# Kernel tuning notes

Hardware: AMD Instinct MI355X
Metric: run time of the kernel (lower is better)

The kernel has to match this reference:

```python
import jax, jax.numpy as jnp
import numpy as np

VOCAB = 50257
D_MODEL = 256
HIDDEN = 512
NUM_CLASSES = 2
BATCH = 64
SEQ = 512
PAD_IDX = 0


def setup_inputs() -> dict:
    key = jax.random.key(0)
    ks = jax.random.split(key, 8)
    input_ids = jax.random.randint(ks[0], (BATCH, SEQ), 0, VOCAB)
    emb = jax.random.normal(ks[1], (VOCAB, D_MODEL), dtype=jnp.float32) * 0.02
    emb = emb.at[PAD_IDX].set(0.0)  # padding_idx row is zero
    s_x = 1.0 / np.sqrt(D_MODEL)
    s_h = 1.0 / np.sqrt(HIDDEN)
    Wx = jax.random.uniform(ks[2], (D_MODEL, 3 * HIDDEN), minval=-s_x, maxval=s_x)
    Wh = jax.random.uniform(ks[3], (HIDDEN, 3 * HIDDEN), minval=-s_h, maxval=s_h)
    bx = jax.random.uniform(ks[4], (3 * HIDDEN,), minval=-s_h, maxval=s_h)
    bh = jax.random.uniform(ks[5], (3 * HIDDEN,), minval=-s_h, maxval=s_h)
    Wo = jax.random.uniform(ks[6], (HIDDEN, NUM_CLASSES), minval=-s_h, maxval=s_h)
    bo = jax.random.uniform(ks[7], (NUM_CLASSES,), minval=-s_h, maxval=s_h)
    return {"input_ids": input_ids, "emb": emb, "Wx": Wx, "Wh": Wh,
            "bx": bx, "bh": bh, "Wo": Wo, "bo": bo}


def reference(input_ids, emb, Wx, Wh, bx, bh, Wo, bo):
    # Embedding lookup: [B, S, D]
    x = emb[input_ids]
    # Precompute input-side gate projections for all timesteps: [B, S, 3H]
    xg = jnp.einsum('bsd,dg->bsg', x, Wx) + bx
    H = Wh.shape[0]
    h0 = jnp.zeros((input_ids.shape[0], H), dtype=x.dtype)

    def step(h, xg_t):
        hg = h @ Wh + bh                    # [B, 3H]
        xr, xz, xn = jnp.split(xg_t, 3, axis=-1)
        hr, hz, hn = jnp.split(hg, 3, axis=-1)
        r = jax.nn.sigmoid(xr + hr)
        z = jax.nn.sigmoid(xz + hz)
        n = jnp.tanh(xn + r * hn)
        h_new = (1.0 - z) * n + z * h
        return h_new, None

    # scan over time; only the last hidden state feeds the classifier head
    h_last, _ = jax.lax.scan(step, h0, jnp.swapaxes(xg, 0, 1))
    # Dropout is identity in eval mode (p=0.5 at train time)
    logits = h_last @ Wo + bo               # [B, num_classes]
    return logits
```

## Files before the change

### kernel.cpp

```cpp
#include <hip/hip_runtime.h>
#include <hip/hip_bf16.h>

#define BATCH   64
#define SEQ     512
#define DMODEL  256
#define HIDDEN  512
#define G3      1536
#define NBLK    128
#define UPB     4
#define CPB     12
#define CHUNK   128
#define NCHUNK  4
#define HSLOT   (HIDDEN * BATCH)

typedef unsigned long long u64;
typedef unsigned int u32;

__global__ __launch_bounds__(512) void prep_wh(const float* __restrict__ Wh,
                                               float* __restrict__ whp) {
    int t = blockIdx.x * 512 + threadIdx.x;
    int k   = t & 511;
    int cb  = t >> 9;
    int c   = cb % 12;
    int blk = cb / 12;
    int u = c & 3, g = c >> 2;
    whp[t] = Wh[(long)k * G3 + g * HIDDEN + blk * UPB + u];
}

__global__ void init_flags(unsigned* flags) {
    __hip_atomic_store(&flags[threadIdx.x], 0u, __ATOMIC_RELAXED,
                       __HIP_MEMORY_SCOPE_AGENT);
}

__global__ __launch_bounds__(256) void xg_gemm(const int* __restrict__ ids,
                                               const float* __restrict__ emb,
                                               const float* __restrict__ Wx,
                                               const float* __restrict__ bx,
                                               float* __restrict__ xgC,
                                               int chunk) {
    __shared__ float Es[64][68];
    __shared__ float Ws[64][68];
    __shared__ int   sids[64];

    const int tid = threadIdx.x;
    const int nb = blockIdx.x;
    const int lt = blockIdx.y;
    const int s  = chunk * CHUNK + lt;
    const int tn = tid & 15;
    const int tm = tid >> 4;

    if (tid < 64) sids[tid] = ids[tid * SEQ + s];
    __syncthreads();

    float acc[4][4];
#pragma unroll
    for (int i = 0; i < 4; ++i)
#pragma unroll
        for (int j = 0; j < 4; ++j) acc[i][j] = 0.f;

    for (int kb = 0; kb < 256; kb += 64) {
#pragma unroll
        for (int p = 0; p < 4; ++p) {
            int b = p * 16 + tm;
            float4 av = *(const float4*)(emb + (long)sids[b] * DMODEL + kb + tn * 4);
            Es[tn * 4 + 0][b] = av.x;
            Es[tn * 4 + 1][b] = av.y;
            Es[tn * 4 + 2][b] = av.z;
            Es[tn * 4 + 3][b] = av.w;
            int krow = p * 16 + tm;
            float4 wv = *(const float4*)(Wx + (long)(kb + krow) * G3 + nb * 64 + tn * 4);
            *(float4*)&Ws[krow][tn * 4] = wv;
        }
        __syncthreads();
#pragma unroll
        for (int k = 0; k < 64; ++k) {
            float4 w4 = *(const float4*)&Ws[k][tm * 4];
            float4 e4 = *(const float4*)&Es[k][tn * 4];
            float ww[4] = {w4.x, w4.y, w4.z, w4.w};
            float ee[4] = {e4.x, e4.y, e4.z, e4.w};
#pragma unroll
            for (int i = 0; i < 4; ++i)
#pragma unroll
                for (int j = 0; j < 4; ++j)
                    acc[i][j] = fmaf(ww[i], ee[j], acc[i][j]);
        }
        __syncthreads();
    }

#pragma unroll
    for (int i = 0; i < 4; ++i) {
        int col = nb * 64 + tm * 4 + i;
        float bxi = bx[col];
        float4 o;
        o.x = acc[i][0] + bxi;
        o.y = acc[i][1] + bxi;
        o.z = acc[i][2] + bxi;
        o.w = acc[i][3] + bxi;
        *(float4*)(xgC + (long)col * (CHUNK * BATCH) + lt * 64 + tn * 4) = o;
    }
}

__global__ __launch_bounds__(512, 2) void gru_scan(const float* __restrict__ whp,
                                                   const float* __restrict__ xgC,
                                                   const float* __restrict__ bh,
                                                   float* hist,
                                                   unsigned* flags,
                                                   int chunk) {
    const int tid = threadIdx.x;
    const int blk = blockIdx.x;
    const int b   = tid & 63;
    const int wu  = __builtin_amdgcn_readfirstlane(tid >> 6);

    __shared__ float part[8][CPB][64];
    __shared__ float hl[UPB][64];

    const float* wb = whp + blk * (CPB * HIDDEN) + wu * 64;
    const int base = chunk * CHUNK;

    const int gu = tid >> 6;
    int jg = 0;
    float bhr = 0.f, bhz = 0.f, bhn = 0.f;
    const float* xr_p = nullptr; const float* xz_p = nullptr; const float* xn_p = nullptr;
    if (tid < 256) {
        jg  = blk * UPB + gu;
        bhr = bh[jg];
        bhz = bh[HIDDEN + jg];
        bhn = bh[2 * HIDDEN + jg];
        xr_p = xgC + (long)jg * (CHUNK * BATCH) + b;
        xz_p = xgC + (long)(HIDDEN + jg) * (CHUNK * BATCH) + b;
        xn_p = xgC + (long)(2 * HIDDEN + jg) * (CHUNK * BATCH) + b;
        hl[gu][b] = (chunk == 0) ? 0.f
                                 : hist[(long)blk * 256 + b * 4 + gu];
    }
    __syncthreads();

#pragma unroll 1
    for (int lt = 0; lt < CHUNK; ++lt) {
        const int t = base + lt;
        const float* hs = hist + (long)lt * HSLOT;
        float*       hw = hist + (long)((lt + 1) & (CHUNK - 1)) * HSLOT;

        float xr = 0.f, xz = 0.f, xn = 0.f, hprev = 0.f;
        if (tid < 256) {
            xr = xr_p[lt * 64];
            xz = xz_p[lt * 64];
            xn = xn_p[lt * 64];
            hprev = hl[gu][b];
        }

        if (t > 0) {
            const float4* hq4 = (const float4*)hs + (wu * 16) * 64 + b;
            float4 hv[16];
#pragma unroll
            for (int i = 0; i < 16; ++i)
                hv[i] = hq4[(long)i * 64];

            float acc[CPB];
#pragma unroll
            for (int c = 0; c < CPB; ++c) acc[c] = 0.f;
#pragma unroll
            for (int i = 0; i < 16; ++i) {
                const float he[4] = {hv[i].x, hv[i].y, hv[i].z, hv[i].w};
#pragma unroll
                for (int e = 0; e < 4; ++e) {
                    const float hvv = he[e];
                    const int kk = i * 4 + e;
#pragma unroll
                    for (int c = 0; c < CPB; ++c)
                        acc[c] = fmaf(hvv, wb[c * HIDDEN + kk], acc[c]);
                }
            }
#pragma unroll
            for (int c = 0; c < CPB; ++c) part[wu][c][b] = acc[c];
        } else {
#pragma unroll
            for (int c = 0; c < CPB; ++c) part[wu][c][b] = 0.f;
        }
        __syncthreads();

        if (tid < 256) {
            float hgr = bhr, hgz = bhz, hgn = bhn;
#pragma unroll
            for (int ww = 0; ww < 8; ++ww) {
                hgr += part[ww][gu][b];
                hgz += part[ww][4 + gu][b];
                hgn += part[ww][8 + gu][b];
            }
            float r  = 1.f / (1.f + expf(-(xr + hgr)));
            float z  = 1.f / (1.f + expf(-(xz + hgz)));
            float nn = tanhf(xn + r * hgn);
            hl[gu][b] = (1.f - z) * nn + z * hprev;
        }
        __syncthreads();

        if (tid < 128) {
            const int p = tid >> 6;
            u32 lo = __float_as_uint(hl[2 * p][b]);
            u32 hi = __float_as_uint(hl[2 * p + 1][b]);
            u64 pk = ((u64)hi << 32) | (u64)lo;
            __hip_atomic_store((u64*)(hw + (long)blk * 256 + b * 4 + 2 * p), pk,
                               __ATOMIC_RELAXED, __HIP_MEMORY_SCOPE_AGENT);
        }

        if (lt < CHUNK - 1) {
            __syncthreads();
            if (tid == 0)
                __hip_atomic_store(&flags[blk], (u32)(t + 1),
                                   __ATOMIC_RELAXED, __HIP_MEMORY_SCOPE_AGENT);
            if (wu == 0) {
                const u32 tgt = (u32)(t + 1);
                for (;;) {
                    u32 f0 = __hip_atomic_load(&flags[b], __ATOMIC_RELAXED,
                                               __HIP_MEMORY_SCOPE_AGENT);
                    u32 f1 = __hip_atomic_load(&flags[64 + b], __ATOMIC_RELAXED,
                                               __HIP_MEMORY_SCOPE_AGENT);
                    if (__all(f0 >= tgt && f1 >= tgt)) break;
                    __builtin_amdgcn_s_sleep(1);
                }
            }
            __syncthreads();
        }
    }
}

__global__ void head_kernel(const float* __restrict__ hist,
                            const float* __restrict__ Wo,
                            const float* __restrict__ bo,
                            float* __restrict__ out) {
    int tid = threadIdx.x;
    int b = tid >> 1, n = tid & 1;
    float acc = bo[n];
#pragma unroll 8
    for (int k = 0; k < HIDDEN; ++k)
        acc = fmaf(hist[(k >> 2) * 256 + b * 4 + (k & 3)], Wo[k * 2 + n], acc);
    out[b * 2 + n] = acc;
}

extern "C" void kernel_launch(void* const* d_in, const int* in_sizes, int n_in,
                              void* d_out, int out_size, void* d_ws, size_t ws_size,
                              hipStream_t stream) {
    (void)in_sizes; (void)n_in; (void)out_size; (void)ws_size;
    const int*   ids = (const int*)  d_in[0];
    const float* emb = (const float*)d_in[1];
    const float* Wx  = (const float*)d_in[2];
    const float* Wh  = (const float*)d_in[3];
    const float* bx  = (const float*)d_in[4];
    const float* bh  = (const float*)d_in[5];
    const float* Wo  = (const float*)d_in[6];
    const float* bo  = (const float*)d_in[7];
    float* out = (float*)d_out;

    char* ws = (char*)d_ws;
    unsigned* flags = (unsigned*)ws;
    float* hist = (float*)(ws + 1024);
    float* whp  = (float*)(ws + 1024 + (size_t)CHUNK * HSLOT * 4);
    float* xgC  = (float*)(ws + 1024 + (size_t)CHUNK * HSLOT * 4
                           + (size_t)NBLK * CPB * HIDDEN * 4);

    init_flags<<<dim3(1), dim3(NBLK), 0, stream>>>(flags);
    prep_wh<<<dim3(1536), dim3(512), 0, stream>>>(Wh, whp);
    for (int c = 0; c < NCHUNK; ++c) {
        xg_gemm<<<dim3(24, CHUNK), dim3(256), 0, stream>>>(ids, emb, Wx, bx, xgC, c);
        gru_scan<<<dim3(NBLK), dim3(512), 0, stream>>>(whp, xgC, bh, hist, flags, c);
    }
    head_kernel<<<dim3(1), dim3(128), 0, stream>>>(hist, Wo, bo, out);
}
```

Before: 5.740 ms.

## Replace per-block barrier with per-unit flags and per-wave consumer waits

The GRU scan drops the block-wide flag barrier. Each hidden unit now publishes its own flag once its h value is stored, and each wave waits only on the 64 units it consumes before loading its slice of h. The partial-sum shared buffer is double-buffered so one __syncthreads per step is enough, hprev lives in registers, and h is stored as plain [unit][batch] instead of packed pairs. This shortens the serial critical path per timestep but adds polling traffic (512 flags) and relies on relaxed atomics plus a vmcnt wait for ordering.

```diff
diff --git a/kernel.cpp b/kernel.cpp
--- a/kernel.cpp
+++ b/kernel.cpp
@@ -111,114 +111,93 @@
     const int b   = tid & 63;
     const int wu  = __builtin_amdgcn_readfirstlane(tid >> 6);
 
-    __shared__ float part[8][CPB][64];
-    __shared__ float hl[UPB][64];
+    __shared__ float part[2][8][CPB][64];
 
     const float* wb = whp + blk * (CPB * HIDDEN) + wu * 64;
     const int base = chunk * CHUNK;
 
-    const int gu = tid >> 6;
     int jg = 0;
-    float bhr = 0.f, bhz = 0.f, bhn = 0.f;
+    float bhr = 0.f, bhz = 0.f, bhn = 0.f, hprev = 0.f;
     const float* xr_p = nullptr; const float* xz_p = nullptr; const float* xn_p = nullptr;
-    if (tid < 256) {
-        jg  = blk * UPB + gu;
+    if (wu < 4) {
+        jg  = blk * UPB + wu;
         bhr = bh[jg];
         bhz = bh[HIDDEN + jg];
         bhn = bh[2 * HIDDEN + jg];
         xr_p = xgC + (long)jg * (CHUNK * BATCH) + b;
         xz_p = xgC + (long)(HIDDEN + jg) * (CHUNK * BATCH) + b;
         xn_p = xgC + (long)(2 * HIDDEN + jg) * (CHUNK * BATCH) + b;
-        hl[gu][b] = (chunk == 0) ? 0.f
-                                 : hist[(long)blk * 256 + b * 4 + gu];
-    }
-    __syncthreads();
+        hprev = (chunk == 0) ? 0.f : hist[(long)jg * 64 + b];
+    }
 
 #pragma unroll 1
     for (int lt = 0; lt < CHUNK; ++lt) {
-        const int t = base + lt;
+        const int t  = base + lt;
+        const int pb = lt & 1;
         const float* hs = hist + (long)lt * HSLOT;
         float*       hw = hist + (long)((lt + 1) & (CHUNK - 1)) * HSLOT;
 
-        float xr = 0.f, xz = 0.f, xn = 0.f, hprev = 0.f;
-        if (tid < 256) {
+        float xr = 0.f, xz = 0.f, xn = 0.f;
+        if (wu < 4) {
             xr = xr_p[lt * 64];
             xz = xz_p[lt * 64];
             xn = xn_p[lt * 64];
-            hprev = hl[gu][b];
-        }
+        }
+
+        float acc[CPB];
+#pragma unroll
+        for (int c = 0; c < CPB; ++c) acc[c] = 0.f;
 
         if (t > 0) {
-            const float4* hq4 = (const float4*)hs + (wu * 16) * 64 + b;
-            float4 hv[16];
-#pragma unroll
-            for (int i = 0; i < 16; ++i)
-                hv[i] = hq4[(long)i * 64];
-
-            float acc[CPB];
-#pragma unroll
-            for (int c = 0; c < CPB; ++c) acc[c] = 0.f;
-#pragma unroll
-            for (int i = 0; i < 16; ++i) {
-                const float he[4] = {hv[i].x, hv[i].y, hv[i].z, hv[i].w};
-#pragma unroll
-                for (int e = 0; e < 4; ++e) {
-                    const float hvv = he[e];
-                    const int kk = i * 4 + e;
-#pragma unroll
-                    for (int c = 0; c < CPB; ++c)
-                        acc[c] = fmaf(hvv, wb[c * HIDDEN + kk], acc[c]);
+            if (lt > 0) {
+                const u32 tgt = (u32)t;
+                for (;;) {
+                    u32 f = __hip_atomic_load(&flags[wu * 64 + b], __ATOMIC_RELAXED,
+                                              __HIP_MEMORY_SCOPE_AGENT);
+                    if (__all((int)(f >= tgt))) break;
+                    __builtin_amdgcn_s_sleep(1);
                 }
             }
-#pragma unroll
-            for (int c = 0; c < CPB; ++c) part[wu][c][b] = acc[c];
-        } else {
-#pragma unroll
-            for (int c = 0; c < CPB; ++c) part[wu][c][b] = 0.f;
-        }
+            const float* hq = hs + (long)wu * (64 * 64) + b;
+            float hv[64];
+#pragma unroll
+            for (int i = 0; i < 64; ++i)
+                hv[i] = hq[i * 64];
+
+#pragma unroll
+            for (int i = 0; i < 64; ++i) {
+                const float hvv = hv[i];
+#pragma unroll
+                for (int c = 0; c < CPB; ++c)
+                    acc[c] = fmaf(hvv, wb[c * HIDDEN + i], acc[c]);
+            }
+        }
+
+#pragma unroll
+        for (int c = 0; c < CPB; ++c) part[pb][wu][c][b] = acc[c];
         __syncthreads();
 
-        if (tid < 256) {
+        if (wu < 4) {
+            __builtin_amdgcn_s_setprio(1);
             float hgr = bhr, hgz = bhz, hgn = bhn;
 #pragma unroll
             for (int ww = 0; ww < 8; ++ww) {
-                hgr += part[ww][gu][b];
-                hgz += part[ww][4 + gu][b];
-                hgn += part[ww][8 + gu][b];
+                hgr += part[pb][ww][wu][b];
+                hgz += part[pb][ww][4 + wu][b];
+                hgn += part[pb][ww][8 + wu][b];
             }
             float r  = 1.f / (1.f + expf(-(xr + hgr)));
             float z  = 1.f / (1.f + expf(-(xz + hgz)));
             float nn = tanhf(xn + r * hgn);
-            hl[gu][b] = (1.f - z) * nn + z * hprev;
-        }
-        __syncthreads();
-
-        if (tid < 128) {
-            const int p = tid >> 6;
-            u32 lo = __float_as_uint(hl[2 * p][b]);
-            u32 hi = __float_as_uint(hl[2 * p + 1][b]);
-            u64 pk = ((u64)hi << 32) | (u64)lo;
-            __hip_atomic_store((u64*)(hw + (long)blk * 256 + b * 4 + 2 * p), pk,
+            float hnew = (1.f - z) * nn + z * hprev;
+            hprev = hnew;
+            __hip_atomic_store((u32*)hw + (long)jg * 64 + b, __float_as_uint(hnew),
                                __ATOMIC_RELAXED, __HIP_MEMORY_SCOPE_AGENT);
-        }
-
-        if (lt < CHUNK - 1) {
-            __syncthreads();
-            if (tid == 0)
-                __hip_atomic_store(&flags[blk], (u32)(t + 1),
-                                   __ATOMIC_RELAXED, __HIP_MEMORY_SCOPE_AGENT);
-            if (wu == 0) {
-                const u32 tgt = (u32)(t + 1);
-                for (;;) {
-                    u32 f0 = __hip_atomic_load(&flags[b], __ATOMIC_RELAXED,
-                                               __HIP_MEMORY_SCOPE_AGENT);
-                    u32 f1 = __hip_atomic_load(&flags[64 + b], __ATOMIC_RELAXED,
-                                               __HIP_MEMORY_SCOPE_AGENT);
-                    if (__all(f0 >= tgt && f1 >= tgt)) break;
-                    __builtin_amdgcn_s_sleep(1);
-                }
-            }
-            __syncthreads();
+            asm volatile("s_waitcnt vmcnt(0)" ::: "memory");
+            if (b == 0)
+                __hip_atomic_store(&flags[jg], (u32)(t + 1), __ATOMIC_RELAXED,
+                                   __HIP_MEMORY_SCOPE_AGENT);
+            __builtin_amdgcn_s_setprio(0);
         }
     }
 }
@@ -232,7 +211,7 @@
     float acc = bo[n];
 #pragma unroll 8
     for (int k = 0; k < HIDDEN; ++k)
-        acc = fmaf(hist[(k >> 2) * 256 + b * 4 + (k & 3)], Wo[k * 2 + n], acc);
+        acc = fmaf(hist[(long)k * 64 + b], Wo[k * 2 + n], acc);
     out[b * 2 + n] = acc;
 }
 
@@ -252,12 +231,12 @@
 
     char* ws = (char*)d_ws;
     unsigned* flags = (unsigned*)ws;
-    float* hist = (float*)(ws + 1024);
-    float* whp  = (float*)(ws + 1024 + (size_t)CHUNK * HSLOT * 4);
-    float* xgC  = (float*)(ws + 1024 + (size_t)CHUNK * HSLOT * 4
+    float* hist = (float*)(ws + 2048);
+    float* whp  = (float*)(ws + 2048 + (size_t)CHUNK * HSLOT * 4);
+    float* xgC  = (float*)(ws + 2048 + (size_t)CHUNK * HSLOT * 4
                            + (size_t)NBLK * CPB * HIDDEN * 4);
 
-    init_flags<<<dim3(1), dim3(NBLK), 0, stream>>>(flags);
+    init_flags<<<dim3(1), dim3(512), 0, stream>>>(flags);
     prep_wh<<<dim3(1536), dim3(512), 0, stream>>>(Wh, whp);
     for (int c = 0; c < NCHUNK; ++c) {
         xg_gemm<<<dim3(24, CHUNK), dim3(256), 0, stream>>>(ids, emb, Wx, bx, xgC, c);
```

After: 5.683 ms. No clear change (-1.0%).
